# Kernel tuning notes

Hardware: AMD Instinct MI355X
Metric: run time of the kernel (lower is better)

The kernel has to match this reference:

```python
import jax, jax.numpy as jnp
import numpy as np

M, N, K, O = 2048, 2048, 64, 128


def setup_inputs() -> dict:
    key = jax.random.key(0)
    k1, k2, k3 = jax.random.split(key, 3)
    adj = (jax.random.uniform(k1, (M, N)) < 0.02).astype(jnp.float32)
    features = jax.random.normal(k2, (N, K), dtype=jnp.float32)
    W = jax.random.normal(k3, (4 * K, O), dtype=jnp.float32) / np.sqrt(4 * K)
    b = jnp.zeros((O,), dtype=jnp.float32)
    return {"adj": adj, "features": features, "W": W, "b": b}


def reference(adj, features, W, b):
    # product[m,n,k] = adj[m,n] * features[n,k]  (faithfully materialized as in torch einsum)
    product = adj[:, :, None] * features[None, :, :]  # (M, N, K)
    mean = product.mean(axis=1)                        # (M, K) -- mean over all N incl. zeros, as in torch
    mx = product.max(axis=1)                           # (M, K)
    mn = product.min(axis=1)                           # (M, K)
    std = jnp.std(product, axis=1, ddof=1)             # torch.std default is unbiased (ddof=1)
    combined = jnp.concatenate([mean, mx, mn, std], axis=1)  # (M, 4K)
    return jnp.tanh(combined @ W + b)                  # (M, O)
```

## Files before the change

kernel.cpp:

```cpp
#include <hip/hip_runtime.h>
#include <math.h>

#define PM 2048
#define PN 2048
#define PK 64
#define PO 128
#define RPB 4
#define NBLK (PM / RPB)
#define CAPL 128

__global__ __launch_bounds__(512, 4) void pna_fused(
    const float* __restrict__ adj,
    const float* __restrict__ feat,
    const float* __restrict__ W,
    const float* __restrict__ b,
    float* __restrict__ out)
{
    __shared__ float red_s [8][PK];
    __shared__ float red_s2[8][PK];
    __shared__ float red_mx[8][PK];
    __shared__ float red_mn[8][PK];
    __shared__ int   red_cnt[8];
    __shared__ int   list[8][CAPL];
    __shared__ float comb[RPB][4 * PK];
    __shared__ float part[RPB][16][PO];

    const int t    = threadIdx.x;
    const int w    = t >> 6;
    const int lane = t & 63;
    const int r    = w >> 1;
    const int h    = w & 1;
    const int m0   = blockIdx.x * RPB;

    const float* adjrow = adj + (size_t)(m0 + r) * PN;
    const int base = h * 1024;

    float4 a[4];
    #pragma unroll
    for (int it = 0; it < 4; ++it)
        a[it] = *reinterpret_cast<const float4*>(adjrow + base + it * 256 + lane * 4);

    const int ol = (t & 31) << 2;
    const int jc = t >> 5;
    float4 wreg[16];
    #pragma unroll
    for (int jj = 0; jj < 16; ++jj)
        wreg[jj] = *reinterpret_cast<const float4*>(W + (size_t)(jc * 16 + jj) * PO + ol);

    const unsigned long long below = (1ULL << lane) - 1ULL;
    int off = 0;
    #pragma unroll
    for (int it = 0; it < 4; ++it) {
        const int c0 = base + it * 256 + lane * 4;
        const float ae[4] = {a[it].x, a[it].y, a[it].z, a[it].w};
        #pragma unroll
        for (int e = 0; e < 4; ++e) {
            const unsigned long long m = __ballot(ae[e] != 0.0f);
            const int p = off + (int)__popcll(m & below);
            if (ae[e] != 0.0f && p < CAPL) list[w][p] = c0 + e;
            off += (int)__popcll(m);
        }
    }
    const int cnt = off;
    const int T = (cnt < CAPL) ? cnt : CAPL;

    float s = 0.0f, s2 = 0.0f;
    float mx = -INFINITY, mn = INFINITY;
    int i = 0;
    for (; i + 8 <= T; i += 8) {
        int   nn[8];
        float v[8];
        #pragma unroll
        for (int u = 0; u < 8; ++u) nn[u] = list[w][i + u];
        #pragma unroll
        for (int u = 0; u < 8; ++u) v[u] = feat[(size_t)nn[u] * PK + lane];
        #pragma unroll
        for (int u = 0; u < 8; ++u) {
            s += v[u]; s2 += v[u] * v[u];
            mx = fmaxf(mx, v[u]); mn = fminf(mn, v[u]);
        }
    }
    for (; i + 4 <= T; i += 4) {
        int nn[4]; float v[4];
        #pragma unroll
        for (int u = 0; u < 4; ++u) nn[u] = list[w][i + u];
        #pragma unroll
        for (int u = 0; u < 4; ++u) v[u] = feat[(size_t)nn[u] * PK + lane];
        #pragma unroll
        for (int u = 0; u < 4; ++u) {
            s += v[u]; s2 += v[u] * v[u];
            mx = fmaxf(mx, v[u]); mn = fminf(mn, v[u]);
        }
    }
    for (; i < T; ++i) {
        const float v = feat[(size_t)list[w][i] * PK + lane];
        s += v; s2 += v * v;
        mx = fmaxf(mx, v); mn = fminf(mn, v);
    }

    red_s [w][lane] = s;
    red_s2[w][lane] = s2;
    red_mx[w][lane] = mx;
    red_mn[w][lane] = mn;
    if (lane == 0) red_cnt[w] = cnt;
    __syncthreads();

    if (t < RPB * PK) {
        const int rr = t >> 6;
        const int k  = t & 63;
        float S = 0.0f, S2 = 0.0f, MX = -INFINITY, MN = INFINITY;
        int C = 0;
        #pragma unroll
        for (int ww = 0; ww < 2; ++ww) {
            S  += red_s [rr * 2 + ww][k];
            S2 += red_s2[rr * 2 + ww][k];
            MX = fmaxf(MX, red_mx[rr * 2 + ww][k]);
            MN = fminf(MN, red_mn[rr * 2 + ww][k]);
            C  += red_cnt[rr * 2 + ww];
        }
        const float mean = S / (float)PN;
        float var = (S2 - S * S / (float)PN) / (float)(PN - 1);
        var = fmaxf(var, 0.0f);
        const float sd = sqrtf(var);
        if (C < PN) { MX = fmaxf(MX, 0.0f); MN = fminf(MN, 0.0f); }
        comb[rr][k]          = mean;
        comb[rr][PK + k]     = MX;
        comb[rr][2 * PK + k] = MN;
        comb[rr][3 * PK + k] = sd;
    }
    __syncthreads();

    {
        float4 acc[RPB];
        #pragma unroll
        for (int rr = 0; rr < RPB; ++rr) acc[rr] = make_float4(0.f, 0.f, 0.f, 0.f);
        #pragma unroll
        for (int jj4 = 0; jj4 < 4; ++jj4) {
            const int j0 = jc * 16 + jj4 * 4;
            float4 c4[RPB];
            #pragma unroll
            for (int rr = 0; rr < RPB; ++rr)
                c4[rr] = *reinterpret_cast<const float4*>(&comb[rr][j0]);
            #pragma unroll
            for (int e = 0; e < 4; ++e) {
                const float4 wv = wreg[jj4 * 4 + e];
                #pragma unroll
                for (int rr = 0; rr < RPB; ++rr) {
                    const float c = (e == 0) ? c4[rr].x : (e == 1) ? c4[rr].y
                                  : (e == 2) ? c4[rr].z : c4[rr].w;
                    acc[rr].x = fmaf(c, wv.x, acc[rr].x);
                    acc[rr].y = fmaf(c, wv.y, acc[rr].y);
                    acc[rr].z = fmaf(c, wv.z, acc[rr].z);
                    acc[rr].w = fmaf(c, wv.w, acc[rr].w);
                }
            }
        }
        #pragma unroll
        for (int rr = 0; rr < RPB; ++rr)
            *reinterpret_cast<float4*>(&part[rr][jc][ol]) = acc[rr];
    }
    __syncthreads();

    {
        const int rr = t >> 7;
        const int o  = t & (PO - 1);
        float v = 0.0f;
        #pragma unroll
        for (int c = 0; c < 16; ++c) v += part[rr][c][o];
        v += b[o];
        out[(size_t)(m0 + rr) * PO + o] = tanhf(v);
    }
}

extern "C" void kernel_launch(void* const* d_in, const int* in_sizes, int n_in,
                              void* d_out, int out_size, void* d_ws, size_t ws_size,
                              hipStream_t stream) {
    const float* adj  = (const float*)d_in[0];
    const float* feat = (const float*)d_in[1];
    const float* W    = (const float*)d_in[2];
    const float* b    = (const float*)d_in[3];
    float* out = (float*)d_out;

    pna_fused<<<NBLK, 512, 0, stream>>>(adj, feat, W, b, out);
}
```

Before: 13.17 us.

## Fuse stat finalization into matvec, drop comb buffer and W register prefetch

```diff
diff --git a/kernel.cpp b/kernel.cpp
--- a/kernel.cpp
+++ b/kernel.cpp
@@ -9,7 +9,7 @@
 #define NBLK (PM / RPB)
 #define CAPL 128
 
-__global__ __launch_bounds__(512, 4) void pna_fused(
+__global__ __launch_bounds__(512) void pna_fused(
     const float* __restrict__ adj,
     const float* __restrict__ feat,
     const float* __restrict__ W,
@@ -22,7 +22,6 @@
     __shared__ float red_mn[8][PK];
     __shared__ int   red_cnt[8];
     __shared__ int   list[8][CAPL];
-    __shared__ float comb[RPB][4 * PK];
     __shared__ float part[RPB][16][PO];
 
     const int t    = threadIdx.x;
@@ -40,13 +39,6 @@
     for (int it = 0; it < 4; ++it)
         a[it] = *reinterpret_cast<const float4*>(adjrow + base + it * 256 + lane * 4);
 
-    const int ol = (t & 31) << 2;
-    const int jc = t >> 5;
-    float4 wreg[16];
-    #pragma unroll
-    for (int jj = 0; jj < 16; ++jj)
-        wreg[jj] = *reinterpret_cast<const float4*>(W + (size_t)(jc * 16 + jj) * PO + ol);
-
     const unsigned long long below = (1ULL << lane) - 1ULL;
     int off = 0;
     #pragma unroll
@@ -105,45 +97,95 @@
     if (lane == 0) red_cnt[w] = cnt;
     __syncthreads();
 
-    if (t < RPB * PK) {
-        const int rr = t >> 6;
-        const int k  = t & 63;
-        float S = 0.0f, S2 = 0.0f, MX = -INFINITY, MN = INFINITY;
-        int C = 0;
-        #pragma unroll
-        for (int ww = 0; ww < 2; ++ww) {
-            S  += red_s [rr * 2 + ww][k];
-            S2 += red_s2[rr * 2 + ww][k];
-            MX = fmaxf(MX, red_mx[rr * 2 + ww][k]);
-            MN = fminf(MN, red_mn[rr * 2 + ww][k]);
-            C  += red_cnt[rr * 2 + ww];
-        }
-        const float mean = S / (float)PN;
-        float var = (S2 - S * S / (float)PN) / (float)(PN - 1);
-        var = fmaxf(var, 0.0f);
-        const float sd = sqrtf(var);
-        if (C < PN) { MX = fmaxf(MX, 0.0f); MN = fminf(MN, 0.0f); }
-        comb[rr][k]          = mean;
-        comb[rr][PK + k]     = MX;
-        comb[rr][2 * PK + k] = MN;
-        comb[rr][3 * PK + k] = sd;
-    }
-    __syncthreads();
-
     {
+        const int jc  = t >> 5;
+        const int ol  = (t & 31) << 2;
+        const int seg = jc >> 2;
+        const int k0  = (jc & 3) << 4;
+
+        const float invN  = 1.0f / (float)PN;
+        const float invN1 = 1.0f / (float)(PN - 1);
+
+        bool clampr[RPB];
+        #pragma unroll
+        for (int rr = 0; rr < RPB; ++rr) {
+            const int C = red_cnt[2 * rr] + red_cnt[2 * rr + 1];
+            clampr[rr] = (C < PN);
+        }
+
         float4 acc[RPB];
         #pragma unroll
         for (int rr = 0; rr < RPB; ++rr) acc[rr] = make_float4(0.f, 0.f, 0.f, 0.f);
+
         #pragma unroll
         for (int jj4 = 0; jj4 < 4; ++jj4) {
-            const int j0 = jc * 16 + jj4 * 4;
+            const int kk = k0 + jj4 * 4;
             float4 c4[RPB];
-            #pragma unroll
-            for (int rr = 0; rr < RPB; ++rr)
-                c4[rr] = *reinterpret_cast<const float4*>(&comb[rr][j0]);
+            if (seg == 0) {
+                #pragma unroll
+                for (int rr = 0; rr < RPB; ++rr) {
+                    const float4 sA = *reinterpret_cast<const float4*>(&red_s[2 * rr][kk]);
+                    const float4 sB = *reinterpret_cast<const float4*>(&red_s[2 * rr + 1][kk]);
+                    c4[rr] = make_float4((sA.x + sB.x) * invN, (sA.y + sB.y) * invN,
+                                         (sA.z + sB.z) * invN, (sA.w + sB.w) * invN);
+                }
+            } else if (seg == 1) {
+                #pragma unroll
+                for (int rr = 0; rr < RPB; ++rr) {
+                    const float4 mA = *reinterpret_cast<const float4*>(&red_mx[2 * rr][kk]);
+                    const float4 mB = *reinterpret_cast<const float4*>(&red_mx[2 * rr + 1][kk]);
+                    float4 c = make_float4(fmaxf(mA.x, mB.x), fmaxf(mA.y, mB.y),
+                                           fmaxf(mA.z, mB.z), fmaxf(mA.w, mB.w));
+                    if (clampr[rr]) {
+                        c.x = fmaxf(c.x, 0.f); c.y = fmaxf(c.y, 0.f);
+                        c.z = fmaxf(c.z, 0.f); c.w = fmaxf(c.w, 0.f);
+                    }
+                    c4[rr] = c;
+                }
+            } else if (seg == 2) {
+                #pragma unroll
+                for (int rr = 0; rr < RPB; ++rr) {
+                    const float4 mA = *reinterpret_cast<const float4*>(&red_mn[2 * rr][kk]);
+                    const float4 mB = *reinterpret_cast<const float4*>(&red_mn[2 * rr + 1][kk]);
+                    float4 c = make_float4(fminf(mA.x, mB.x), fminf(mA.y, mB.y),
+                                           fminf(mA.z, mB.z), fminf(mA.w, mB.w));
+                    if (clampr[rr]) {
+                        c.x = fminf(c.x, 0.f); c.y = fminf(c.y, 0.f);
+                        c.z = fminf(c.z, 0.f); c.w = fminf(c.w, 0.f);
+                    }
+                    c4[rr] = c;
+                }
+            } else {
+                #pragma unroll
+                for (int rr = 0; rr < RPB; ++rr) {
+                    const float4 sA  = *reinterpret_cast<const float4*>(&red_s [2 * rr][kk]);
+                    const float4 sB  = *reinterpret_cast<const float4*>(&red_s [2 * rr + 1][kk]);
+                    const float4 qA  = *reinterpret_cast<const float4*>(&red_s2[2 * rr][kk]);
+                    const float4 qB  = *reinterpret_cast<const float4*>(&red_s2[2 * rr + 1][kk]);
+                    float4 c;
+                    {
+                        const float S = sA.x + sB.x, Q = qA.x + qB.x;
+                        c.x = sqrtf(fmaxf((Q - S * S * invN) * invN1, 0.f));
+                    }
+                    {
+                        const float S = sA.y + sB.y, Q = qA.y + qB.y;
+                        c.y = sqrtf(fmaxf((Q - S * S * invN) * invN1, 0.f));
+                    }
+                    {
+                        const float S = sA.z + sB.z, Q = qA.z + qB.z;
+                        c.z = sqrtf(fmaxf((Q - S * S * invN) * invN1, 0.f));
+                    }
+                    {
+                        const float S = sA.w + sB.w, Q = qA.w + qB.w;
+                        c.w = sqrtf(fmaxf((Q - S * S * invN) * invN1, 0.f));
+                    }
+                    c4[rr] = c;
+                }
+            }
             #pragma unroll
             for (int e = 0; e < 4; ++e) {
-                const float4 wv = wreg[jj4 * 4 + e];
+                const int j = jc * 16 + jj4 * 4 + e;
+                const float4 wv = *reinterpret_cast<const float4*>(W + (size_t)j * PO + ol);
                 #pragma unroll
                 for (int rr = 0; rr < RPB; ++rr) {
                     const float c = (e == 0) ? c4[rr].x : (e == 1) ? c4[rr].y
```

Result: slower. 21.76 us (+65.3%).
